# Kernel tuning notes

Hardware: AMD Instinct MI355X
Metric: run time of the kernel (lower is better)

## Reference

```python
import jax, jax.numpy as jnp
import numpy as np

NUM_HEADS = 16


def _mhsa(x, Wq, Wk, Wv, Wo):
    B, S, D = x.shape
    H = NUM_HEADS
    dk = D // H
    # Linear applies weight [out, in]: y = x @ W.T
    Q = jnp.einsum('bsd,ed->bse', x, Wq).reshape(B, S, H, dk).transpose(0, 2, 1, 3)
    K = jnp.einsum('bsd,ed->bse', x, Wk).reshape(B, S, H, dk).transpose(0, 2, 1, 3)
    V = jnp.einsum('bsd,ed->bse', x, Wv).reshape(B, S, H, dk).transpose(0, 2, 1, 3)
    scores = jnp.einsum('bhqd,bhkd->bhqk', Q, K) / jnp.sqrt(jnp.asarray(dk, x.dtype))
    causal = jnp.tril(jnp.ones((S, S), dtype=bool))  # True = keep
    scores = jnp.where(causal, scores, jnp.asarray(-jnp.inf, x.dtype))
    attn = jax.nn.softmax(scores, axis=-1)
    out = jnp.einsum('bhqk,bhkd->bhqd', attn, V)  # [B,H,S,dk]
    out = out.transpose(0, 2, 1, 3).reshape(B, S, D)
    return jnp.einsum('bsd,ed->bse', out, Wo)


def setup_inputs() -> dict:
    key = jax.random.key(0)
    ks = jax.random.split(key, 5)
    B, S, D = 4, 2048, 1024
    std = 2.0 / (D + D) ** 0.5
    return {
        'x': jax.random.normal(ks[0], (B, S, D), dtype=jnp.float32),
        'Wq': jax.random.normal(ks[1], (D, D), dtype=jnp.float32) * std,
        'Wk': jax.random.normal(ks[2], (D, D), dtype=jnp.float32) * std,
        'Wv': jax.random.normal(ks[3], (D, D), dtype=jnp.float32) * std,
        'Wo': jax.random.normal(ks[4], (D, D), dtype=jnp.float32) * std,
    }


def reference(x, Wq, Wk, Wv, Wo):
    return _mhsa(x, Wq, Wk, Wv, Wo)
```

## Files before the change

kernel.cpp:

```cpp
#include <hip/hip_runtime.h>
#include <hip/hip_bf16.h>
#include <stdint.h>

typedef __attribute__((ext_vector_type(8))) short short8;
typedef __attribute__((ext_vector_type(4))) float f32x4;

static __device__ __forceinline__ void gload_lds16(const void* g, void* l) {
  __builtin_amdgcn_global_load_lds((const __attribute__((address_space(1))) void*)g,
                                   (__attribute__((address_space(3))) void*)l,
                                   16, 0, 0);
}

static __device__ __forceinline__ unsigned short f2bf(float f) {
  union { __hip_bfloat16 h; unsigned short s; } u;
  u.h = __float2bfloat16(f);
  return u.s;
}

#define WAIT4_BARRIER() asm volatile("s_waitcnt vmcnt(4) lgkmcnt(0)\n\ts_barrier" ::: "memory")
#define WAIT0_BARRIER() asm volatile("s_waitcnt vmcnt(0) lgkmcnt(0)\n\ts_barrier" ::: "memory")

__global__ void cast_all(const float* __restrict__ x, const float* __restrict__ Wq,
                         const float* __restrict__ Wk, const float* __restrict__ Wv,
                         const float* __restrict__ Wo,
                         unsigned short* __restrict__ xb, unsigned short* __restrict__ Wqb,
                         unsigned short* __restrict__ Wkb, unsigned short* __restrict__ Wvb,
                         unsigned short* __restrict__ Wob) {
  const int i = blockIdx.x * 256 + threadIdx.x;
  const float* src;
  unsigned short* dst;
  int off;
  if (i < 2097152) {
    src = x; dst = xb; off = i;
  } else {
    const int j = i - 2097152;
    const int wsel = j >> 18;
    off = j & 262143;
    src = wsel == 0 ? Wq : wsel == 1 ? Wk : wsel == 2 ? Wv : Wo;
    dst = wsel == 0 ? Wqb : wsel == 1 ? Wkb : wsel == 2 ? Wvb : Wob;
  }
  float4 v = reinterpret_cast<const float4*>(src)[off];
  ushort4 o;
  o.x = f2bf(v.x); o.y = f2bf(v.y); o.z = f2bf(v.z); o.w = f2bf(v.w);
  reinterpret_cast<ushort4*>(dst)[off] = o;
}

template <typename OutT>
static __device__ __forceinline__ void gemm_tile(const unsigned short* __restrict__ A,
                                                 const unsigned short* __restrict__ B,
                                                 OutT* __restrict__ C,
                                                 int brow, int bcol, int ldc,
                                                 short* sA, short* sB) {
  const int t = threadIdx.x;
  const int w = t >> 6, l = t & 63, lg = l >> 4, lr = l & 15;
  const int wr = w >> 1, wc = w & 1;

  f32x4 acc[4][4] = {};

  auto stage = [&](int buf, int kt) {
#pragma unroll
    for (int r = 0; r < 2; ++r) {
      const int byteoff = t * 16 + r * 4096;
      const int row = byteoff >> 6;
      const int inrow = (byteoff & 63) ^ (((row >> 1) & 3) << 4);
      gload_lds16((const char*)A + ((size_t)(brow + row) * 1024 + kt) * 2 + inrow,
                  (char*)(sA + buf * 4096) + byteoff);
      gload_lds16((const char*)B + ((size_t)(bcol + row) * 1024 + kt) * 2 + inrow,
                  (char*)(sB + buf * 4096) + byteoff);
    }
  };

  stage(0, 0);
  stage(1, 32);
  int cur = 0;

  for (int kti = 0; kti < 32; ++kti) {
    if (kti < 31) WAIT4_BARRIER();
    else         WAIT0_BARRIER();
    if (kti + 2 < 32) {
      int b2 = cur + 2; if (b2 >= 3) b2 -= 3;
      stage(b2, (kti + 2) << 5);
    }
    const char* sAc = (const char*)(sA + cur * 4096);
    const char* sBc = (const char*)(sB + cur * 4096);

    short8 af[4], bfr[4];
#pragma unroll
    for (int m = 0; m < 4; ++m) {
      const int arow = wr * 64 + m * 16 + lr;
      af[m] = *reinterpret_cast<const short8*>(
          sAc + arow * 64 + ((lg * 16) ^ (((arow >> 1) & 3) << 4)));
    }
#pragma unroll
    for (int n = 0; n < 4; ++n) {
      const int brw = wc * 64 + n * 16 + lr;
      bfr[n] = *reinterpret_cast<const short8*>(
          sBc + brw * 64 + ((lg * 16) ^ (((brw >> 1) & 3) << 4)));
    }
    __builtin_amdgcn_s_setprio(1);
#pragma unroll
    for (int m = 0; m < 4; ++m)
#pragma unroll
      for (int n = 0; n < 4; ++n)
        acc[m][n] = __builtin_amdgcn_mfma_f32_16x16x32_bf16(af[m], bfr[n], acc[m][n], 0, 0, 0);
    __builtin_amdgcn_s_setprio(0);

    ++cur; if (cur == 3) cur = 0;
  }

#pragma unroll
  for (int m = 0; m < 4; ++m) {
#pragma unroll
    for (int n = 0; n < 4; ++n) {
#pragma unroll
      for (int j = 0; j < 4; ++j) {
        const int rr = brow + wr * 64 + m * 16 + lg * 4 + j;
        const int cc = bcol + wc * 64 + n * 16 + lr;
        if constexpr (sizeof(OutT) == 2) {
          C[(size_t)rr * ldc + cc] = (OutT)f2bf(acc[m][n][j]);
        } else {
          C[(size_t)rr * ldc + cc] = acc[m][n][j];
        }
      }
    }
  }
}

__global__ __launch_bounds__(256) void gemm_qkv(const unsigned short* __restrict__ xb,
                                                const unsigned short* __restrict__ Wqb,
                                                const unsigned short* __restrict__ Wkb,
                                                const unsigned short* __restrict__ Wvb,
                                                unsigned short* __restrict__ Qb,
                                                unsigned short* __restrict__ Kb,
                                                unsigned short* __restrict__ Vt) {
  __shared__ short sA[3][4096];
  __shared__ short sB[3][4096];
  const int i = blockIdx.x;
  const int lid = (i & 7) * 192 + (i >> 3);
  const int z = lid >> 9, r = lid & 511;

  const unsigned short *A, *B;
  unsigned short* C;
  int brow, bcol, ldc;
  if (z == 2) {
    A = Wvb; B = xb; C = Vt;
    brow = (r & 7) << 7; bcol = (r >> 3) << 7; ldc = 8192;
  } else {
    A = xb; B = z ? Wkb : Wqb; C = z ? Kb : Qb;
    brow = (r >> 3) << 7; bcol = (r & 7) << 7; ldc = 1024;
  }
  gemm_tile<unsigned short>(A, B, C, brow, bcol, ldc, sA[0], sB[0]);
}

__global__ __launch_bounds__(256) void gemm_out(const unsigned short* __restrict__ AO,
                                                const unsigned short* __restrict__ Wob,
                                                float* __restrict__ out) {
  __shared__ short sA[3][4096];
  __shared__ short sB[3][4096];
  const int i = blockIdx.x;
  const int lid = (i & 7) * 64 + (i >> 3);
  gemm_tile<float>(AO, Wob, out, (lid >> 3) << 7, (lid & 7) << 7, 1024, sA[0], sB[0]);
}

__global__ __launch_bounds__(256) void attn_kernel(const unsigned short* __restrict__ Qg,
                                                   const unsigned short* __restrict__ Kg,
                                                   const unsigned short* __restrict__ Vtg,
                                                   unsigned short* __restrict__ AO) {
  const int S = 2048, D = 1024, SN = 8192;
  const int i = blockIdx.x;
  const int lid = (i & 7) * 128 + (i >> 3);
  const int qp = lid & 15;
  const int bh = lid >> 4;
  const int b = bh >> 4, h = bh & 15;
  const int t = threadIdx.x;
  const int w = t >> 6, l = t & 63, lg = l >> 4, lr = l & 15;

  __shared__ short sK[3][4096];
  __shared__ short sV[3][4096];
  __shared__ short sP[4096];

  int sboff[2], slin[2], srow[2];
#pragma unroll
  for (int r = 0; r < 2; ++r) {
    sboff[r] = t * 16 + r * 4096;
    srow[r] = sboff[r] >> 7;
    slin[r] = (sboff[r] & 127) ^ ((srow[r] & 7) << 4);
  }
  const char* Kbase = (const char*)Kg + ((size_t)(b * S) * D + h * 64) * 2;
  const char* Vbase = (const char*)Vtg + ((size_t)(h * 64) * SN + (size_t)b * S) * 2;

  const int nkv0 = qp + 1;
  const int qt1 = 31 - qp;

  auto stage = [&](int buf, int j) {
    const int kvt = (j < nkv0) ? j : j - nkv0;
    const size_t kv0 = (size_t)kvt * 64;
#pragma unroll
    for (int r = 0; r < 2; ++r) {
      gload_lds16(Kbase + (kv0 + srow[r]) * 2048 + slin[r],
                  (char*)sK + buf * 8192 + sboff[r]);
      gload_lds16(Vbase + (size_t)srow[r] * 16384 + kv0 * 2 + slin[r],
                  (char*)sV + buf * 8192 + sboff[r]);
    }
  };
  auto load_qf = [&](int qt, short8* qf) {
    const unsigned short* qbase =
        Qg + (size_t)(b * S + qt * 64 + w * 16 + lr) * D + h * 64;
    qf[0] = *reinterpret_cast<const short8*>(qbase + lg * 8);
    qf[1] = *reinterpret_cast<const short8*>(qbase + 32 + lg * 8);
  };

  const float SCL = 0.125f * 1.44269504089f;

  short8 qf[2];
  load_qf(qp, qf);
  stage(0, 0);
  stage(1, 1);

  f32x4 o[4] = {};
  float m = -INFINITY, lsum = 0.f;
  int cur = 0;

  auto epilogue = [&](int qt) {
    const float inv = 1.f / lsum;
    unsigned short* orow = AO + (size_t)(b * S + qt * 64 + w * 16 + lr) * D + h * 64;
#pragma unroll
    for (int dn = 0; dn < 4; ++dn) {
      ushort4 ov;
      ov.x = f2bf(o[dn][0] * inv); ov.y = f2bf(o[dn][1] * inv);
      ov.z = f2bf(o[dn][2] * inv); ov.w = f2bf(o[dn][3] * inv);
      *reinterpret_cast<ushort4*>(orow + dn * 16 + lg * 4) = ov;
    }
  };

#pragma unroll 1
  for (int j = 0; j < 33; ++j) {
    const bool h1 = (j >= nkv0);
    const int kvt = h1 ? j - nkv0 : j;
    const int qt = h1 ? qt1 : qp;

    if (j < 32) WAIT4_BARRIER();
    else        WAIT0_BARRIER();
    if (j + 2 < 33) {
      int b2 = cur + 2; if (b2 >= 3) b2 -= 3;
      stage(b2, j + 2);
    }

    const char* sKc = (const char*)sK + cur * 8192;
    const char* sVc = (const char*)sV + cur * 8192;

    f32x4 sc[4] = {};
    __builtin_amdgcn_s_setprio(1);
#pragma unroll
    for (int n = 0; n < 4; ++n) {
#pragma unroll
      for (int kk = 0; kk < 2; ++kk) {
        const int row = n * 16 + lr;
        const short8 kf = *reinterpret_cast<const short8*>(
            sKc + (row << 7) + ((kk * 64 + lg * 16) ^ ((row & 7) << 4)));
        sc[n] = __builtin_amdgcn_mfma_f32_16x16x32_bf16(kf, qf[kk], sc[n], 0, 0, 0);
      }
    }
    __builtin_amdgcn_s_setprio(0);

    float p[4][4];
    const bool diag = (kvt == qt);
    const int ql = w * 16 + lr;
#pragma unroll
    for (int n = 0; n < 4; ++n) {
#pragma unroll
      for (int r = 0; r < 4; ++r) {
        float v = sc[n][r] * SCL;
        if (diag && (n * 16 + lg * 4 + r) > ql) v = -INFINITY;
        p[n][r] = v;
      }
    }

    float mx = p[0][0];
#pragma unroll
    for (int n = 0; n < 4; ++n)
#pragma unroll
      for (int r = 0; r < 4; ++r) mx = fmaxf(mx, p[n][r]);
    mx = fmaxf(mx, __shfl_xor(mx, 16));
    mx = fmaxf(mx, __shfl_xor(mx, 32));
    if (!__all(mx <= m + 8.0f)) {
      const float mnew = fmaxf(m, mx);
      const float alpha = __builtin_amdgcn_exp2f(m - mnew);
      m = mnew;
      lsum *= alpha;
#pragma unroll
      for (int dn = 0; dn < 4; ++dn) o[dn] *= alpha;
    }

    float s = 0.f;
#pragma unroll
    for (int n = 0; n < 4; ++n) {
#pragma unroll
      for (int r = 0; r < 4; ++r) {
        const float e = __builtin_amdgcn_exp2f(p[n][r] - m);
        p[n][r] = e;
        s += e;
      }
    }
    s += __shfl_xor(s, 16);
    s += __shfl_xor(s, 32);
    lsum += s;

#pragma unroll
    for (int n = 0; n < 4; ++n) {
      ushort4 pk;
      pk.x = f2bf(p[n][0]); pk.y = f2bf(p[n][1]);
      pk.z = f2bf(p[n][2]); pk.w = f2bf(p[n][3]);
      *reinterpret_cast<ushort4*>(
          (char*)sP + (w << 11) + (lr << 7) + ((n * 32 + lg * 8) ^ ((lr & 7) << 4))) = pk;
    }

    __builtin_amdgcn_s_setprio(1);
#pragma unroll
    for (int kk = 0; kk < 2; ++kk) {
      const short8 pa = *reinterpret_cast<const short8*>(
          (const char*)sP + (w << 11) + (lr << 7) +
          ((kk * 64 + lg * 16) ^ ((lr & 7) << 4)));
#pragma unroll
      for (int dn = 0; dn < 4; ++dn) {
        const int vrow = dn * 16 + lr;
        const short8 vb = *reinterpret_cast<const short8*>(
            sVc + (vrow << 7) + ((kk * 64 + lg * 16) ^ ((vrow & 7) << 4)));
        o[dn] = __builtin_amdgcn_mfma_f32_16x16x32_bf16(vb, pa, o[dn], 0, 0, 0);
      }
    }
    __builtin_amdgcn_s_setprio(0);

    if (j == nkv0 - 1) {
      epilogue(qp);
#pragma unroll
      for (int dn = 0; dn < 4; ++dn) o[dn] = f32x4{0.f, 0.f, 0.f, 0.f};
      m = -INFINITY; lsum = 0.f;
      load_qf(qt1, qf);
    }

    ++cur; if (cur == 3) cur = 0;
  }
  epilogue(qt1);
}

extern "C" void kernel_launch(void* const* d_in, const int* in_sizes, int n_in,
                              void* d_out, int out_size, void* d_ws, size_t ws_size,
                              hipStream_t stream) {
  const float* x  = (const float*)d_in[0];
  const float* Wq = (const float*)d_in[1];
  const float* Wk = (const float*)d_in[2];
  const float* Wv = (const float*)d_in[3];
  const float* Wo = (const float*)d_in[4];
  float* out = (float*)d_out;

  char* ws = (char*)d_ws;
  unsigned short* xb  = (unsigned short*)(ws);
  unsigned short* Wqb = (unsigned short*)(ws + 16777216);
  unsigned short* Wkb = (unsigned short*)(ws + 18874368);
  unsigned short* Wvb = (unsigned short*)(ws + 20971520);
  unsigned short* Wob = (unsigned short*)(ws + 23068672);
  unsigned short* Qb  = (unsigned short*)(ws + 25165824);
  unsigned short* Kb  = (unsigned short*)(ws + 41943040);
  unsigned short* Vt  = (unsigned short*)(ws + 58720256);
  unsigned short* AO  = (unsigned short*)(ws + 75497472);

  cast_all<<<12288, 256, 0, stream>>>(x, Wq, Wk, Wv, Wo, xb, Wqb, Wkb, Wvb, Wob);
  gemm_qkv<<<1536, 256, 0, stream>>>(xb, Wqb, Wkb, Wvb, Qb, Kb, Vt);
  attn_kernel<<<1024, 256, 0, stream>>>(Qb, Kb, Vt, AO);
  gemm_out<<<512, 256, 0, stream>>>(AO, Wob, out);
}
```

Measured before the change: 274.0 us.

## Fold softmax scale into Q projection and switch attention to double-buffered KV

The Q projection epilogue now multiplies by the softmax scale times log2(e), so the attention kernel no longer scales each score. The attention kernel's K/V staging goes from triple buffering with prefetch distance two to double buffering with a full wait-and-barrier at the end of each iteration. The second Q tile's fragments are also preloaded up front instead of being loaded at the switch point. This cuts LDS use and per-element VALU work, but exposes more memory latency because only one tile is in flight and every iteration waits for vmcnt(0).

```diff
diff --git a/kernel.cpp b/kernel.cpp
--- a/kernel.cpp
+++ b/kernel.cpp
@@ -50,7 +50,7 @@
                                                  const unsigned short* __restrict__ B,
                                                  OutT* __restrict__ C,
                                                  int brow, int bcol, int ldc,
-                                                 short* sA, short* sB) {
+                                                 short* sA, short* sB, float oscale) {
   const int t = threadIdx.x;
   const int w = t >> 6, l = t & 63, lg = l >> 4, lr = l & 15;
   const int wr = w >> 1, wc = w & 1;
@@ -117,9 +117,9 @@
         const int rr = brow + wr * 64 + m * 16 + lg * 4 + j;
         const int cc = bcol + wc * 64 + n * 16 + lr;
         if constexpr (sizeof(OutT) == 2) {
-          C[(size_t)rr * ldc + cc] = (OutT)f2bf(acc[m][n][j]);
+          C[(size_t)rr * ldc + cc] = (OutT)f2bf(acc[m][n][j] * oscale);
         } else {
-          C[(size_t)rr * ldc + cc] = acc[m][n][j];
+          C[(size_t)rr * ldc + cc] = acc[m][n][j] * oscale;
         }
       }
     }
@@ -142,14 +142,16 @@
   const unsigned short *A, *B;
   unsigned short* C;
   int brow, bcol, ldc;
+  float oscale = 1.0f;
   if (z == 2) {
     A = Wvb; B = xb; C = Vt;
     brow = (r & 7) << 7; bcol = (r >> 3) << 7; ldc = 8192;
   } else {
     A = xb; B = z ? Wkb : Wqb; C = z ? Kb : Qb;
     brow = (r >> 3) << 7; bcol = (r & 7) << 7; ldc = 1024;
-  }
-  gemm_tile<unsigned short>(A, B, C, brow, bcol, ldc, sA[0], sB[0]);
+    if (z == 0) oscale = 0.125f * 1.44269504089f;
+  }
+  gemm_tile<unsigned short>(A, B, C, brow, bcol, ldc, sA[0], sB[0], oscale);
 }
 
 __global__ __launch_bounds__(256) void gemm_out(const unsigned short* __restrict__ AO,
@@ -159,7 +161,8 @@
   __shared__ short sB[3][4096];
   const int i = blockIdx.x;
   const int lid = (i & 7) * 64 + (i >> 3);
-  gemm_tile<float>(AO, Wob, out, (lid >> 3) << 7, (lid & 7) << 7, 1024, sA[0], sB[0]);
+  gemm_tile<float>(AO, Wob, out, (lid >> 3) << 7, (lid & 7) << 7, 1024,
+                   sA[0], sB[0], 1.0f);
 }
 
 __global__ __launch_bounds__(256) void attn_kernel(const unsigned short* __restrict__ Qg,
@@ -175,8 +178,8 @@
   const int t = threadIdx.x;
   const int w = t >> 6, l = t & 63, lg = l >> 4, lr = l & 15;
 
-  __shared__ short sK[3][4096];
-  __shared__ short sV[3][4096];
+  __shared__ short sK[2][4096];
+  __shared__ short sV[2][4096];
   __shared__ short sP[4096];
 
   int sboff[2], slin[2], srow[2];
@@ -210,12 +213,10 @@
     qf[1] = *reinterpret_cast<const short8*>(qbase + 32 + lg * 8);
   };
 
-  const float SCL = 0.125f * 1.44269504089f;
-
-  short8 qf[2];
+  short8 qf[2], qfB[2];
   load_qf(qp, qf);
+  load_qf(qt1, qfB);
   stage(0, 0);
-  stage(1, 1);
 
   f32x4 o[4] = {};
   float m = -INFINITY, lsum = 0.f;
@@ -233,18 +234,15 @@
     }
   };
 
+  WAIT0_BARRIER();
+
 #pragma unroll 1
   for (int j = 0; j < 33; ++j) {
     const bool h1 = (j >= nkv0);
     const int kvt = h1 ? j - nkv0 : j;
     const int qt = h1 ? qt1 : qp;
 
-    if (j < 32) WAIT4_BARRIER();
-    else        WAIT0_BARRIER();
-    if (j + 2 < 33) {
-      int b2 = cur + 2; if (b2 >= 3) b2 -= 3;
-      stage(b2, j + 2);
-    }
+    if (j + 1 < 33) stage(cur ^ 1, j + 1);
 
     const char* sKc = (const char*)sK + cur * 8192;
     const char* sVc = (const char*)sV + cur * 8192;
@@ -263,24 +261,20 @@
     }
     __builtin_amdgcn_s_setprio(0);
 
-    float p[4][4];
-    const bool diag = (kvt == qt);
-    const int ql = w * 16 + lr;
-#pragma unroll
-    for (int n = 0; n < 4; ++n) {
-#pragma unroll
-      for (int r = 0; r < 4; ++r) {
-        float v = sc[n][r] * SCL;
-        if (diag && (n * 16 + lg * 4 + r) > ql) v = -INFINITY;
-        p[n][r] = v;
-      }
-    }
-
-    float mx = p[0][0];
+    if (kvt == qt) {
+      const int ql = w * 16 + lr;
+#pragma unroll
+      for (int n = 0; n < 4; ++n)
+#pragma unroll
+        for (int r = 0; r < 4; ++r)
+          if ((n * 16 + lg * 4 + r) > ql) sc[n][r] = -INFINITY;
+    }
+
+    float mx = sc[0][0];
 #pragma unroll
     for (int n = 0; n < 4; ++n)
 #pragma unroll
-      for (int r = 0; r < 4; ++r) mx = fmaxf(mx, p[n][r]);
+      for (int r = 0; r < 4; ++r) mx = fmaxf(mx, sc[n][r]);
     mx = fmaxf(mx, __shfl_xor(mx, 16));
     mx = fmaxf(mx, __shfl_xor(mx, 32));
     if (!__all(mx <= m + 8.0f)) {
@@ -292,12 +286,13 @@
       for (int dn = 0; dn < 4; ++dn) o[dn] *= alpha;
     }
 
+    float p[4][4];
     float s = 0.f;
 #pragma unroll
     for (int n = 0; n < 4; ++n) {
 #pragma unroll
       for (int r = 0; r < 4; ++r) {
-        const float e = __builtin_amdgcn_exp2f(p[n][r] - m);
+        const float e = __builtin_amdgcn_exp2f(sc[n][r] - m);
         p[n][r] = e;
         s += e;
       }
@@ -336,10 +331,11 @@
 #pragma unroll
       for (int dn = 0; dn < 4; ++dn) o[dn] = f32x4{0.f, 0.f, 0.f, 0.f};
       m = -INFINITY; lsum = 0.f;
-      load_qf(qt1, qf);
-    }
-
-    ++cur; if (cur == 3) cur = 0;
+      qf[0] = qfB[0]; qf[1] = qfB[1];
+    }
+
+    if (j + 1 < 33) WAIT0_BARRIER();
+    cur ^= 1;
   }
   epilogue(qt1);
 }
```

New measurement: 254.1 us. 7.3% less time.
